# Kernel tuning notes

Hardware: AMD Instinct MI355X
Metric: run time of the kernel (lower is better)

## Reference

```python
import jax, jax.numpy as jnp
import numpy as np

S = 14
B = 2
C = 20
LAMBDA_COORD = 5.0
LAMBDA_NOOBJ = 0.5
BATCH = 4096


def setup_inputs() -> dict:
    key = jax.random.key(0)
    k1, k2, k3 = jax.random.split(key, 3)
    pred = jax.random.uniform(k1, (BATCH, S, S, B * 5 + C), dtype=jnp.float32)
    target = jax.random.uniform(k2, (BATCH, S, S, B * 5 + C), dtype=jnp.float32)
    obj = (jax.random.uniform(k3, (BATCH, S, S), dtype=jnp.float32) < 0.15).astype(jnp.float32)
    target = target.at[..., 4].set(obj)
    target = target.at[..., 9].set(obj)
    return {"pred": pred, "target": target}


def _iou(box1, box2):
    # box1, box2: (..., 4) = [x, y, w, h]; elementwise IoU over leading dims
    b1x1 = box1[..., 0] - box1[..., 2] / 2
    b1y1 = box1[..., 1] - box1[..., 3] / 2
    b1x2 = box1[..., 0] + box1[..., 2] / 2
    b1y2 = box1[..., 1] + box1[..., 3] / 2
    b2x1 = box2[..., 0] - box2[..., 2] / 2
    b2y1 = box2[..., 1] - box2[..., 3] / 2
    b2x2 = box2[..., 0] + box2[..., 2] / 2
    b2y2 = box2[..., 1] + box2[..., 3] / 2
    iw = jnp.clip(jnp.minimum(b1x2, b2x2) - jnp.maximum(b1x1, b2x1), 0)
    ih = jnp.clip(jnp.minimum(b1y2, b2y2) - jnp.maximum(b1y1, b2y1), 0)
    inter = iw * ih
    a1 = (b1x2 - b1x1) * (b1y2 - b1y1)
    a2 = (b2x2 - b2x1) * (b2y2 - b2y1)
    return inter / (a1 + a2 - inter + 1e-6)


def reference(pred, target):
    bs = pred.shape[0]
    tb = target[..., : B * 5].reshape(bs, S, S, B, 5)
    pb = pred[..., : B * 5].reshape(bs, S, S, B, 5)
    tcls = target[..., B * 5 :]
    pcls = pred[..., B * 5 :]

    obj_mask = tb[..., 4] > 0          # (bs,S,S,B)
    has_obj = obj_mask[..., 0]         # (bs,S,S)
    noobj_mask = ~obj_mask

    # no-object confidence loss over every non-obj box slot
    conf_err2 = (pb[..., 4] - tb[..., 4]) ** 2
    noobj_loss = jnp.sum(jnp.where(noobj_mask, conf_err2, 0.0))

    # per-box IoU between i-th pred box and i-th target box in each cell
    ious = _iou(pb[..., :4], tb[..., :4])            # (bs,S,S,B)
    best_idx = jnp.argmax(ious, axis=-1)             # (bs,S,S)
    idx = best_idx[..., None, None]
    p_best = jnp.take_along_axis(pb, idx, axis=3)[..., 0, :]  # (bs,S,S,5)
    t_best = jnp.take_along_axis(tb, idx, axis=3)[..., 0, :]

    m = has_obj                                       # (bs,S,S) bool
    mf = m.astype(pred.dtype)

    xy_loss = jnp.sum(mf[..., None] * (p_best[..., :2] - t_best[..., :2]) ** 2)
    p_wh = jnp.sqrt(jnp.abs(p_best[..., 2:4]) + 1e-6)
    t_wh_safe = jnp.where(m[..., None], t_best[..., 2:4], 1.0)  # avoid sqrt(0) grad NaN
    t_wh = jnp.sqrt(t_wh_safe)
    wh_loss = jnp.sum(mf[..., None] * (p_wh - t_wh) ** 2)
    coord_loss = xy_loss + wh_loss

    obj_loss = jnp.sum(mf * (p_best[..., 4] - t_best[..., 4]) ** 2)

    # non-best box confidence pushed to 0 (B=2: the other slot)
    nonbest_conf = jnp.sum(pb[..., 4], axis=-1) - p_best[..., 4]
    noobj_loss = noobj_loss + LAMBDA_NOOBJ * jnp.sum(mf * nonbest_conf ** 2)

    class_loss = jnp.sum(mf[..., None] * (pcls - tcls) ** 2)

    total = LAMBDA_COORD * coord_loss + obj_loss + LAMBDA_NOOBJ * noobj_loss + class_loss
    return total / bs
```

## Files before the change

### kernel.cpp

```cpp
#include <hip/hip_runtime.h>


#define FEAT 30
#define CELLS 802816
#define TPB 256
#define CPB 256
#define NBLOCKS (CELLS / CPB)
#define F4_PER_ARRAY (CPB * FEAT / 4)

typedef float f32x4 __attribute__((ext_vector_type(4)));

__device__ __forceinline__ float iou_f(float x1, float y1, float w1, float h1,
                                       float x2, float y2, float w2, float h2) {
    float b1x1 = x1 - 0.5f * w1, b1x2 = x1 + 0.5f * w1;
    float b1y1 = y1 - 0.5f * h1, b1y2 = y1 + 0.5f * h1;
    float b2x1 = x2 - 0.5f * w2, b2x2 = x2 + 0.5f * w2;
    float b2y1 = y2 - 0.5f * h2, b2y2 = y2 + 0.5f * h2;
    float iw = fmaxf(fminf(b1x2, b2x2) - fmaxf(b1x1, b2x1), 0.0f);
    float ih = fmaxf(fminf(b1y2, b2y2) - fmaxf(b1y1, b2y1), 0.0f);
    float inter = iw * ih;
    float a1 = (b1x2 - b1x1) * (b1y2 - b1y1);
    float a2 = (b2x2 - b2x1) * (b2y2 - b2y1);
    return inter / (a1 + a2 - inter + 1e-6f);
}

__global__ __launch_bounds__(TPB, 4) void yolo_main_kernel(
        const float* __restrict__ pred, const float* __restrict__ tgt,
        float* __restrict__ partials) {
    __shared__ float sb[CPB * FEAT];
    __shared__ float wave_sum[TPB / 64];

    const int tid = threadIdx.x;
    const long long base = (long long)blockIdx.x * (CPB * FEAT);
    const bool tail = tid < (F4_PER_ARRAY - 7 * TPB);

    const f32x4* gp = (const f32x4*)(pred + base);
    const f32x4* gt = (const f32x4*)(tgt + base);
    f32x4* l = (f32x4*)sb;

    f32x4 pr[8], tr[8];
#pragma unroll
    for (int i = 0; i < 7; ++i)
        pr[i] = __builtin_nontemporal_load(&gp[tid + i * TPB]);
    if (tail) pr[7] = __builtin_nontemporal_load(&gp[tid + 7 * TPB]);
#pragma unroll
    for (int i = 0; i < 7; ++i)
        tr[i] = __builtin_nontemporal_load(&gt[tid + i * TPB]);
    if (tail) tr[7] = __builtin_nontemporal_load(&gt[tid + 7 * TPB]);
    __builtin_amdgcn_sched_barrier(0);

#pragma unroll
    for (int i = 0; i < 7; ++i) l[tid + i * TPB] = pr[i];
    if (tail) l[tid + 7 * TPB] = pr[7];
    __syncthreads();

    float p[FEAT];
    {
        const float2* pc = (const float2*)(sb + tid * FEAT);
#pragma unroll
        for (int i = 0; i < FEAT / 2; ++i) {
            float2 v = pc[i];
            p[2 * i] = v.x;
            p[2 * i + 1] = v.y;
        }
    }
    __syncthreads();

#pragma unroll
    for (int i = 0; i < 7; ++i) l[tid + i * TPB] = tr[i];
    if (tail) l[tid + 7 * TPB] = tr[7];
    __syncthreads();

    const float2* tc = (const float2*)(sb + tid * FEAT);
    float t[10];
#pragma unroll
    for (int i = 0; i < 5; ++i) {
        float2 v = tc[i];
        t[2 * i] = v.x;
        t[2 * i + 1] = v.y;
    }

    const bool obj0 = t[4] > 0.0f;
    const bool obj1 = t[9] > 0.0f;
    const float mf = obj0 ? 1.0f : 0.0f;

    float d0 = p[4] - t[4];
    float d1 = p[9] - t[9];
    float noobj = (obj0 ? 0.0f : d0 * d0) + (obj1 ? 0.0f : d1 * d1);

    float iou0 = iou_f(p[0], p[1], p[2], p[3], t[0], t[1], t[2], t[3]);
    float iou1 = iou_f(p[5], p[6], p[7], p[8], t[5], t[6], t[7], t[8]);
    const bool sel1 = iou1 > iou0;

    float pbx = sel1 ? p[5] : p[0];
    float pby = sel1 ? p[6] : p[1];
    float pbw = sel1 ? p[7] : p[2];
    float pbh = sel1 ? p[8] : p[3];
    float pbc = sel1 ? p[9] : p[4];
    float tbx = sel1 ? t[5] : t[0];
    float tby = sel1 ? t[6] : t[1];
    float tbw = sel1 ? t[7] : t[2];
    float tbh = sel1 ? t[8] : t[3];
    float tbc = sel1 ? t[9] : t[4];

    float dx = pbx - tbx, dy = pby - tby;
    float xy = dx * dx + dy * dy;

    float pw = sqrtf(fabsf(pbw) + 1e-6f);
    float ph = sqrtf(fabsf(pbh) + 1e-6f);
    float tw = sqrtf(obj0 ? tbw : 1.0f);
    float th = sqrtf(obj0 ? tbh : 1.0f);
    float dw = pw - tw, dh = ph - th;
    float wh = dw * dw + dh * dh;

    float dc = pbc - tbc;
    float obj_l = dc * dc;

    float nonbest = (p[4] + p[9]) - pbc;
    noobj += 0.5f * mf * nonbest * nonbest;

    float cls = 0.0f;
#pragma unroll
    for (int i = 5; i < FEAT / 2; ++i) {
        float2 v = tc[i];
        float da = p[2 * i] - v.x;
        float db = p[2 * i + 1] - v.y;
        cls += da * da + db * db;
    }

    float cell = 5.0f * mf * (xy + wh) + mf * obj_l + 0.5f * noobj + mf * cls;

    float v = cell;
#pragma unroll
    for (int off = 32; off > 0; off >>= 1) v += __shfl_down(v, off, 64);
    if ((tid & 63) == 0) wave_sum[tid >> 6] = v;
    __syncthreads();
    if (tid == 0)
        partials[blockIdx.x] = wave_sum[0] + wave_sum[1] + wave_sum[2] + wave_sum[3];
}

__global__ __launch_bounds__(TPB) void yolo_reduce_kernel(
        const float* __restrict__ partials, float* __restrict__ out) {
    __shared__ float wave_sum[TPB / 64];
    const int tid = threadIdx.x;
    float v = 0.0f;
    for (int i = tid; i < NBLOCKS; i += TPB) v += partials[i];
#pragma unroll
    for (int off = 32; off > 0; off >>= 1) v += __shfl_down(v, off, 64);
    if ((tid & 63) == 0) wave_sum[tid >> 6] = v;
    __syncthreads();
    if (tid == 0)
        out[0] = (wave_sum[0] + wave_sum[1] + wave_sum[2] + wave_sum[3]) *
                 (1.0f / 4096.0f);
}

extern "C" void kernel_launch(void* const* d_in, const int* in_sizes, int n_in,
                              void* d_out, int out_size, void* d_ws, size_t ws_size,
                              hipStream_t stream) {
    const float* pred = (const float*)d_in[0];
    const float* tgt  = (const float*)d_in[1];
    float* out = (float*)d_out;
    float* partials = (float*)d_ws;

    yolo_main_kernel<<<NBLOCKS, TPB, 0, stream>>>(pred, tgt, partials);
    yolo_reduce_kernel<<<1, TPB, 0, stream>>>(partials, out);
}
```

Before: 189.1 us.

## Use persistent blocks with double-buffered LDS and register prefetch of next tile

Switches from one block per 256-cell tile to 512 persistent blocks that each process 6 or 7 tiles. The loads for the next tile are issued into registers while the current tile is computed from double-buffered LDS, so global memory latency overlaps with compute. LDS use per block grows about fourfold (about 120 KB), which limits occupancy to a single block per CU. The scheme relies on raw s_barrier plus waitcnt, and only 512 blocks may underuse the 256 CUs.

```diff
diff --git a/kernel.cpp b/kernel.cpp
--- a/kernel.cpp
+++ b/kernel.cpp
@@ -5,8 +5,9 @@
 #define CELLS 802816
 #define TPB 256
 #define CPB 256
-#define NBLOCKS (CELLS / CPB)
-#define F4_PER_ARRAY (CPB * FEAT / 4)
+#define NTILES (CELLS / CPB)
+#define NBLK 512
+#define F4T (CPB * FEAT / 4)
 
 typedef float f32x4 __attribute__((ext_vector_type(4)));
 
@@ -24,119 +25,130 @@
     return inter / (a1 + a2 - inter + 1e-6f);
 }
 
-__global__ __launch_bounds__(TPB, 4) void yolo_main_kernel(
+__global__ __launch_bounds__(TPB, 2) void yolo_main_kernel(
         const float* __restrict__ pred, const float* __restrict__ tgt,
         float* __restrict__ partials) {
-    __shared__ float sb[CPB * FEAT];
+    __shared__ float sbP[2][CPB * FEAT];
+    __shared__ float sbT[2][CPB * FEAT];
     __shared__ float wave_sum[TPB / 64];
 
-    const int tid = threadIdx.x;
-    const long long base = (long long)blockIdx.x * (CPB * FEAT);
-    const bool tail = tid < (F4_PER_ARRAY - 7 * TPB);
-
-    const f32x4* gp = (const f32x4*)(pred + base);
-    const f32x4* gt = (const f32x4*)(tgt + base);
-    f32x4* l = (f32x4*)sb;
+    const int tid  = threadIdx.x;
+    const int b    = blockIdx.x;
+    const bool tail = tid < (F4T - 7 * TPB);
+    const int t0  = (b < 64) ? b * 7 : 448 + (b - 64) * 6;
+    const int ntl = (b < 64) ? 7 : 6;
 
     f32x4 pr[8], tr[8];
+
+    auto issue = [&](int k) {
+        const f32x4* gp = (const f32x4*)pred + (long long)(t0 + k) * F4T;
+        const f32x4* gt = (const f32x4*)tgt  + (long long)(t0 + k) * F4T;
 #pragma unroll
-    for (int i = 0; i < 7; ++i)
-        pr[i] = __builtin_nontemporal_load(&gp[tid + i * TPB]);
-    if (tail) pr[7] = __builtin_nontemporal_load(&gp[tid + 7 * TPB]);
+        for (int i = 0; i < 7; ++i)
+            pr[i] = __builtin_nontemporal_load(&gp[tid + i * TPB]);
+        if (tail) pr[7] = __builtin_nontemporal_load(&gp[tid + 7 * TPB]);
 #pragma unroll
-    for (int i = 0; i < 7; ++i)
-        tr[i] = __builtin_nontemporal_load(&gt[tid + i * TPB]);
-    if (tail) tr[7] = __builtin_nontemporal_load(&gt[tid + 7 * TPB]);
-    __builtin_amdgcn_sched_barrier(0);
+        for (int i = 0; i < 7; ++i)
+            tr[i] = __builtin_nontemporal_load(&gt[tid + i * TPB]);
+        if (tail) tr[7] = __builtin_nontemporal_load(&gt[tid + 7 * TPB]);
+    };
 
+    issue(0);
+
+    for (int k = 0; k < ntl; ++k) {
+        const int pp = k & 1;
+
+        {
+            f32x4* lp = (f32x4*)sbP[pp];
+            f32x4* lt = (f32x4*)sbT[pp];
 #pragma unroll
-    for (int i = 0; i < 7; ++i) l[tid + i * TPB] = pr[i];
-    if (tail) l[tid + 7 * TPB] = pr[7];
-    __syncthreads();
+            for (int i = 0; i < 7; ++i) lp[tid + i * TPB] = pr[i];
+            if (tail) lp[tid + 7 * TPB] = pr[7];
+#pragma unroll
+            for (int i = 0; i < 7; ++i) lt[tid + i * TPB] = tr[i];
+            if (tail) lt[tid + 7 * TPB] = tr[7];
+        }
+        asm volatile("s_waitcnt lgkmcnt(0)" ::: "memory");
+        __builtin_amdgcn_sched_barrier(0);
+        __builtin_amdgcn_s_barrier();
+        __builtin_amdgcn_sched_barrier(0);
 
-    float p[FEAT];
-    {
-        const float2* pc = (const float2*)(sb + tid * FEAT);
+        if (k + 1 < ntl) issue(k + 1);
+
+        const float2* pc = (const float2*)(sbP[pp] + tid * FEAT);
+        const float2* tc = (const float2*)(sbT[pp] + tid * FEAT);
+        float p[FEAT], t[10];
 #pragma unroll
         for (int i = 0; i < FEAT / 2; ++i) {
-            float2 v = pc[i];
-            p[2 * i] = v.x;
-            p[2 * i + 1] = v.y;
+            float2 v = pc[i]; p[2 * i] = v.x; p[2 * i + 1] = v.y;
         }
+#pragma unroll
+        for (int i = 0; i < 5; ++i) {
+            float2 v = tc[i]; t[2 * i] = v.x; t[2 * i + 1] = v.y;
+        }
+
+        const bool obj0 = t[4] > 0.0f;
+        const bool obj1 = t[9] > 0.0f;
+        const float mf = obj0 ? 1.0f : 0.0f;
+
+        float d0 = p[4] - t[4];
+        float d1 = p[9] - t[9];
+        float noobj = (obj0 ? 0.0f : d0 * d0) + (obj1 ? 0.0f : d1 * d1);
+
+        float iou0 = iou_f(p[0], p[1], p[2], p[3], t[0], t[1], t[2], t[3]);
+        float iou1 = iou_f(p[5], p[6], p[7], p[8], t[5], t[6], t[7], t[8]);
+        const bool sel1 = iou1 > iou0;
+
+        float pbx = sel1 ? p[5] : p[0];
+        float pby = sel1 ? p[6] : p[1];
+        float pbw = sel1 ? p[7] : p[2];
+        float pbh = sel1 ? p[8] : p[3];
+        float pbc = sel1 ? p[9] : p[4];
+        float tbx = sel1 ? t[5] : t[0];
+        float tby = sel1 ? t[6] : t[1];
+        float tbw = sel1 ? t[7] : t[2];
+        float tbh = sel1 ? t[8] : t[3];
+        float tbc = sel1 ? t[9] : t[4];
+
+        float dx = pbx - tbx, dy = pby - tby;
+        float xy = dx * dx + dy * dy;
+
+        float pw = sqrtf(fabsf(pbw) + 1e-6f);
+        float ph = sqrtf(fabsf(pbh) + 1e-6f);
+        float tw = sqrtf(obj0 ? tbw : 1.0f);
+        float th = sqrtf(obj0 ? tbh : 1.0f);
+        float dw = pw - tw, dh = ph - th;
+        float wh = dw * dw + dh * dh;
+
+        float dc = pbc - tbc;
+        float obj_l = dc * dc;
+
+        float nonbest = (p[4] + p[9]) - pbc;
+        noobj += 0.5f * mf * nonbest * nonbest;
+
+        float cls = 0.0f;
+#pragma unroll
+        for (int i = 5; i < FEAT / 2; ++i) {
+            float2 v = tc[i];
+            float da = p[2 * i] - v.x;
+            float db = p[2 * i + 1] - v.y;
+            cls += da * da + db * db;
+        }
+
+        float cell = 5.0f * mf * (xy + wh) + mf * obj_l + 0.5f * noobj + mf * cls;
+
+        float v = cell;
+#pragma unroll
+        for (int off = 32; off > 0; off >>= 1) v += __shfl_down(v, off, 64);
+        if ((tid & 63) == 0) wave_sum[tid >> 6] = v;
+        asm volatile("s_waitcnt lgkmcnt(0)" ::: "memory");
+        __builtin_amdgcn_sched_barrier(0);
+        __builtin_amdgcn_s_barrier();
+        __builtin_amdgcn_sched_barrier(0);
+        if (tid == 0)
+            partials[t0 + k] =
+                wave_sum[0] + wave_sum[1] + wave_sum[2] + wave_sum[3];
     }
-    __syncthreads();
-
-#pragma unroll
-    for (int i = 0; i < 7; ++i) l[tid + i * TPB] = tr[i];
-    if (tail) l[tid + 7 * TPB] = tr[7];
-    __syncthreads();
-
-    const float2* tc = (const float2*)(sb + tid * FEAT);
-    float t[10];
-#pragma unroll
-    for (int i = 0; i < 5; ++i) {
-        float2 v = tc[i];
-        t[2 * i] = v.x;
-        t[2 * i + 1] = v.y;
-    }
-
-    const bool obj0 = t[4] > 0.0f;
-    const bool obj1 = t[9] > 0.0f;
-    const float mf = obj0 ? 1.0f : 0.0f;
-
-    float d0 = p[4] - t[4];
-    float d1 = p[9] - t[9];
-    float noobj = (obj0 ? 0.0f : d0 * d0) + (obj1 ? 0.0f : d1 * d1);
-
-    float iou0 = iou_f(p[0], p[1], p[2], p[3], t[0], t[1], t[2], t[3]);
-    float iou1 = iou_f(p[5], p[6], p[7], p[8], t[5], t[6], t[7], t[8]);
-    const bool sel1 = iou1 > iou0;
-
-    float pbx = sel1 ? p[5] : p[0];
-    float pby = sel1 ? p[6] : p[1];
-    float pbw = sel1 ? p[7] : p[2];
-    float pbh = sel1 ? p[8] : p[3];
-    float pbc = sel1 ? p[9] : p[4];
-    float tbx = sel1 ? t[5] : t[0];
-    float tby = sel1 ? t[6] : t[1];
-    float tbw = sel1 ? t[7] : t[2];
-    float tbh = sel1 ? t[8] : t[3];
-    float tbc = sel1 ? t[9] : t[4];
-
-    float dx = pbx - tbx, dy = pby - tby;
-    float xy = dx * dx + dy * dy;
-
-    float pw = sqrtf(fabsf(pbw) + 1e-6f);
-    float ph = sqrtf(fabsf(pbh) + 1e-6f);
-    float tw = sqrtf(obj0 ? tbw : 1.0f);
-    float th = sqrtf(obj0 ? tbh : 1.0f);
-    float dw = pw - tw, dh = ph - th;
-    float wh = dw * dw + dh * dh;
-
-    float dc = pbc - tbc;
-    float obj_l = dc * dc;
-
-    float nonbest = (p[4] + p[9]) - pbc;
-    noobj += 0.5f * mf * nonbest * nonbest;
-
-    float cls = 0.0f;
-#pragma unroll
-    for (int i = 5; i < FEAT / 2; ++i) {
-        float2 v = tc[i];
-        float da = p[2 * i] - v.x;
-        float db = p[2 * i + 1] - v.y;
-        cls += da * da + db * db;
-    }
-
-    float cell = 5.0f * mf * (xy + wh) + mf * obj_l + 0.5f * noobj + mf * cls;
-
-    float v = cell;
-#pragma unroll
-    for (int off = 32; off > 0; off >>= 1) v += __shfl_down(v, off, 64);
-    if ((tid & 63) == 0) wave_sum[tid >> 6] = v;
-    __syncthreads();
-    if (tid == 0)
-        partials[blockIdx.x] = wave_sum[0] + wave_sum[1] + wave_sum[2] + wave_sum[3];
 }
 
 __global__ __launch_bounds__(TPB) void yolo_reduce_kernel(
@@ -144,7 +156,7 @@
     __shared__ float wave_sum[TPB / 64];
     const int tid = threadIdx.x;
     float v = 0.0f;
-    for (int i = tid; i < NBLOCKS; i += TPB) v += partials[i];
+    for (int i = tid; i < NTILES; i += TPB) v += partials[i];
 #pragma unroll
     for (int off = 32; off > 0; off >>= 1) v += __shfl_down(v, off, 64);
     if ((tid & 63) == 0) wave_sum[tid >> 6] = v;
@@ -162,6 +174,6 @@
     float* out = (float*)d_out;
     float* partials = (float*)d_ws;
 
-    yolo_main_kernel<<<NBLOCKS, TPB, 0, stream>>>(pred, tgt, partials);
+    yolo_main_kernel<<<NBLK, TPB, 0, stream>>>(pred, tgt, partials);
     yolo_reduce_kernel<<<1, TPB, 0, stream>>>(partials, out);
 }
```

New measurement: 191.4 us. About the same (+1.2%).
